# Performance work log

Measured on AMD Instinct MI355X. Metric: run time of the kernel, lower is better.

Reference implementation:

```python
import jax, jax.numpy as jnp
import numpy as np


def setup_inputs() -> dict:
    key = jax.random.key(0)
    k1, k2, k3, k4, k5 = jax.random.split(key, 5)
    B, D_IN, D_OUT = 8192, 4096, 4096
    inp = jax.random.normal(k1, (B, D_IN), dtype=jnp.float32)
    # dir_loc: kaiming-like init then row-normalized (as in __init__)
    dir_loc = jax.random.normal(k2, (D_OUT, D_IN), dtype=jnp.float32) * np.sqrt(2.0 / D_IN)
    dir_loc = dir_loc / jnp.sqrt(jnp.sum(dir_loc ** 2, axis=-1, keepdims=True))
    # raw (softplus-inverse) concentration parameter
    dir_conc_raw = jax.random.uniform(k3, (D_OUT,), dtype=jnp.float32) + 3.0
    # rad_layer = nn.Linear(in, out): default torch init ~ U(-1/sqrt(in), 1/sqrt(in))
    bound = 1.0 / np.sqrt(D_IN)
    rad_w = jax.random.uniform(k4, (D_OUT, D_IN), minval=-bound, maxval=bound, dtype=jnp.float32)
    rad_b = jax.random.uniform(k5, (D_OUT,), minval=-bound, maxval=bound, dtype=jnp.float32)
    bias = jnp.zeros((D_OUT,), dtype=jnp.float32)  # initialized uniform(0,0)
    return {"input": inp, "dir_loc": dir_loc, "dir_conc_raw": dir_conc_raw,
            "rad_w": rad_w, "rad_b": rad_b, "bias": bias}


def reference(input, dir_loc, dir_conc_raw, rad_w, rad_b, bias):
    # sample=False path: direction_sample = PowerSpherical(loc, kappa).mean
    #   = loc * kappa / (kappa + dim - 1), kappa = softplus(raw)
    d = dir_loc.shape[1]
    kappa = jax.nn.softplus(dir_conc_raw)                      # [O]
    direction = dir_loc * (kappa / (kappa + (d - 1)))[:, None]  # [O, I]
    # radius = softplus(Linear(input))
    radius = jax.nn.softplus(input @ rad_w.T + rad_b)          # [B, O]
    # (input.unsqueeze(1) * (direction * radius[..., None])).sum(-1) + bias
    # == (input @ direction.T) * radius + bias  (GEMM + elementwise scale)
    return (input @ direction.T) * radius + bias
```

## Files before the change

### kernel.cpp

```cpp
#include <hip/hip_runtime.h>
#include <hip/hip_bf16.h>
#include <math.h>


typedef __bf16 bf16x8 __attribute__((ext_vector_type(8)));
typedef float  f32x4  __attribute__((ext_vector_type(4)));
typedef unsigned short u16;
typedef u16   u16x4 __attribute__((ext_vector_type(4)));
typedef float f4    __attribute__((ext_vector_type(4)));

#define BDIM 8192
#define IDIM 4096
#define ODIM 4096
#define BM 256
#define BN 128
#define BK 32
#define NKT (IDIM/BK)

__device__ __forceinline__ u16 f2bf(float x){ __bf16 h=(__bf16)x; return __builtin_bit_cast(u16,h); }
__device__ __forceinline__ float bf2f(u16 u){ return (float)__builtin_bit_cast(__bf16,u); }

__global__ void k_scale(const float* __restrict__ raw, float* __restrict__ scale){
  int o = blockIdx.x*256 + threadIdx.x;
  if(o < ODIM){
    float x = raw[o];
    float k = (x > 20.f) ? x : log1pf(expf(x));
    scale[o] = k / (k + (float)(IDIM-1));
  }
}

__global__ void k_split(const f4* __restrict__ src, u16x4* __restrict__ hi,
                        u16x4* __restrict__ lo, int n4){
  int i = blockIdx.x*blockDim.x + threadIdx.x;
  int stride = gridDim.x*blockDim.x;
  for(; i<n4; i+=stride){
    f4 v = src[i];
    u16x4 h, l;
    #pragma unroll
    for(int j=0;j<4;++j){
      float x = v[j];
      u16 hb = f2bf(x);
      h[j] = hb;
      l[j] = f2bf(x - bf2f(hb));
    }
    hi[i]=h; lo[i]=l;
  }
}

__global__ void k_split_dir(const f4* __restrict__ src, const float* __restrict__ scale,
                            u16x4* __restrict__ hi, u16x4* __restrict__ lo, int n4){
  int i = blockIdx.x*blockDim.x + threadIdx.x;
  int stride = gridDim.x*blockDim.x;
  for(; i<n4; i+=stride){
    float s = scale[i>>10];
    f4 v = src[i];
    u16x4 h, l;
    #pragma unroll
    for(int j=0;j<4;++j){
      float x = v[j]*s;
      u16 hb = f2bf(x);
      h[j] = hb;
      l[j] = f2bf(x - bf2f(hb));
    }
    hi[i]=h; lo[i]=l;
  }
}

__device__ __forceinline__ void async16(const u16* g, u16* l){
  __builtin_amdgcn_global_load_lds((const __attribute__((address_space(1))) void*)g,
                                   (__attribute__((address_space(3))) void*)l, 16, 0, 0);
}

__global__ __launch_bounds__(512,2) void k_gemm(
    const u16* __restrict__ Ah, const u16* __restrict__ Al,
    const u16* __restrict__ Rh, const u16* __restrict__ Rl,
    const u16* __restrict__ Dh, const u16* __restrict__ Dl,
    const float* __restrict__ rad_b, const float* __restrict__ bias,
    float* __restrict__ out)
{
  __shared__ __align__(16) u16 smem[2*32768];

  const int tid  = threadIdx.x;
  const int lane = tid & 63;
  const int wid  = tid >> 6;
  const int wr = wid >> 1, wc = wid & 1;

  const int bid = blockIdx.x;
  const int swz = (bid & 7)*128 + (bid >> 3);
  const int bm = swz >> 5;
  const int bn = swz & 31;

  const int r0   = tid >> 2;
  const int cxor = (r0 >> 1) & 3;
  const int c0   = ((tid & 3) ^ cxor) * 8;
  const size_t arow = (size_t)(bm*BM + r0)*IDIM + c0;
  const size_t brow = (size_t)(bn*BN + r0)*IDIM + c0;
  const u16* gAh = Ah + arow;  const u16* gAl = Al + arow;
  const u16* gRh = Rh + brow;  const u16* gRl = Rl + brow;
  const u16* gDh = Dh + brow;  const u16* gDl = Dl + brow;
  u16* dst = smem + tid*8;

  const int lr   = lane & 15;
  const int koff = (((lane >> 4) ^ ((lr >> 1) & 3))) * 8;
  const int aoff = (wr*64 + lr)*BK + koff;
  const int boff = (wc*64 + lr)*BK + koff;

  f32x4 accR[4][4] = {};
  f32x4 accD[4][4] = {};

#define STAGE(BUF, KT) { \
    const int _ko = (KT)*BK; \
    u16* _d = dst + (BUF)*32768; \
    async16(gAh + _ko,            _d);         \
    async16(gAh + 128*IDIM + _ko, _d + 4096);  \
    async16(gAl + _ko,            _d + 8192);  \
    async16(gAl + 128*IDIM + _ko, _d + 12288); \
    async16(gRh + _ko,            _d + 16384); \
    async16(gRl + _ko,            _d + 20480); \
    async16(gDh + _ko,            _d + 24576); \
    async16(gDl + _ko,            _d + 28672); \
  }

#define COMPUTE(BUF) { \
    const u16* sb = smem + (BUF)*32768; \
    bf16x8 ah[4], al[4], bh[4], bl[4]; \
    _Pragma("unroll") for(int mi=0;mi<4;++mi){ \
      ah[mi] = *(const bf16x8*)(sb +        aoff + mi*512); \
      al[mi] = *(const bf16x8*)(sb + 8192 + aoff + mi*512); } \
    _Pragma("unroll") for(int ni=0;ni<4;++ni){ \
      bh[ni] = *(const bf16x8*)(sb + 16384 + boff + ni*512); \
      bl[ni] = *(const bf16x8*)(sb + 20480 + boff + ni*512); } \
    __builtin_amdgcn_s_setprio(1); \
    _Pragma("unroll") for(int mi=0;mi<4;++mi) \
      _Pragma("unroll") for(int ni=0;ni<4;++ni){ \
        accR[mi][ni] = __builtin_amdgcn_mfma_f32_16x16x32_bf16(ah[mi], bh[ni], accR[mi][ni],0,0,0); \
        accR[mi][ni] = __builtin_amdgcn_mfma_f32_16x16x32_bf16(ah[mi], bl[ni], accR[mi][ni],0,0,0); \
        accR[mi][ni] = __builtin_amdgcn_mfma_f32_16x16x32_bf16(al[mi], bh[ni], accR[mi][ni],0,0,0); } \
    __builtin_amdgcn_s_setprio(0); \
    _Pragma("unroll") for(int ni=0;ni<4;++ni){ \
      bh[ni] = *(const bf16x8*)(sb + 24576 + boff + ni*512); \
      bl[ni] = *(const bf16x8*)(sb + 28672 + boff + ni*512); } \
    __builtin_amdgcn_s_setprio(1); \
    _Pragma("unroll") for(int mi=0;mi<4;++mi) \
      _Pragma("unroll") for(int ni=0;ni<4;++ni){ \
        accD[mi][ni] = __builtin_amdgcn_mfma_f32_16x16x32_bf16(ah[mi], bh[ni], accD[mi][ni],0,0,0); \
        accD[mi][ni] = __builtin_amdgcn_mfma_f32_16x16x32_bf16(ah[mi], bl[ni], accD[mi][ni],0,0,0); \
        accD[mi][ni] = __builtin_amdgcn_mfma_f32_16x16x32_bf16(al[mi], bh[ni], accD[mi][ni],0,0,0); } \
    __builtin_amdgcn_s_setprio(0); \
  }

#define K_ITER(BUF, VM, DOSTAGE, NEXTK) { \
    asm volatile("s_waitcnt vmcnt(" VM ")" ::: "memory"); \
    __builtin_amdgcn_s_barrier(); \
    __builtin_amdgcn_sched_barrier(0); \
    COMPUTE(BUF); \
    asm volatile("s_waitcnt lgkmcnt(0)" ::: "memory"); \
    __builtin_amdgcn_sched_barrier(0); \
    __builtin_amdgcn_s_barrier(); \
    if (DOSTAGE) { STAGE(BUF, NEXTK) } \
    __builtin_amdgcn_sched_barrier(0); \
  }

  STAGE(0, 0)
  STAGE(1, 1)
  #pragma unroll 1
  for(int t=0; t<NKT-2; t+=2){
    K_ITER(0, "8", true, t+2)
    K_ITER(1, "8", true, t+3)
  }
  K_ITER(0, "8", false, 0)
  K_ITER(1, "0", false, 0)

#undef K_ITER
#undef COMPUTE
#undef STAGE

  const int orow0 = bm*BM + wr*64 + (lane>>4)*4;
  const int ocol0 = bn*BN + wc*64 + (lane & 15);
  #pragma unroll
  for(int ni=0;ni<4;++ni){
    const int col = ocol0 + ni*16;
    const float rb = rad_b[col];
    const float bs = bias[col];
    #pragma unroll
    for(int mi=0;mi<4;++mi){
      const int row = orow0 + mi*16;
      #pragma unroll
      for(int j=0;j<4;++j){
        float s  = accR[mi][ni][j] + rb;
        float sp = (s > 20.f) ? s : log1pf(expf(s));
        out[(size_t)(row+j)*ODIM + col] = accD[mi][ni][j]*sp + bs;
      }
    }
  }
}

extern "C" void kernel_launch(void* const* d_in, const int* in_sizes, int n_in,
                              void* d_out, int out_size, void* d_ws, size_t ws_size,
                              hipStream_t stream){
  (void)in_sizes; (void)n_in; (void)out_size; (void)ws_size;
  const float* inp  = (const float*)d_in[0];
  const float* dirl = (const float*)d_in[1];
  const float* draw = (const float*)d_in[2];
  const float* radw = (const float*)d_in[3];
  const float* radb = (const float*)d_in[4];
  const float* bias = (const float*)d_in[5];
  float* out = (float*)d_out;

  char* ws = (char*)d_ws;
  u16* Ah = (u16*)(ws);
  u16* Al = (u16*)(ws +  67108864L);
  u16* Rh = (u16*)(ws + 134217728L);
  u16* Rl = (u16*)(ws + 167772160L);
  u16* Dh = (u16*)(ws + 201326592L);
  u16* Dl = (u16*)(ws + 234881024L);
  float* scale = (float*)(ws + 268435456L);

  k_scale<<<dim3(ODIM/256), dim3(256), 0, stream>>>(draw, scale);

  const int n4A = BDIM*IDIM/4;
  const int n4W = ODIM*IDIM/4;
  k_split<<<dim3(2048), dim3(256), 0, stream>>>((const f4*)inp,  (u16x4*)Ah, (u16x4*)Al, n4A);
  k_split<<<dim3(2048), dim3(256), 0, stream>>>((const f4*)radw, (u16x4*)Rh, (u16x4*)Rl, n4W);
  k_split_dir<<<dim3(2048), dim3(256), 0, stream>>>((const f4*)dirl, scale, (u16x4*)Dh, (u16x4*)Dl, n4W);

  k_gemm<<<dim3((BDIM/BM)*(ODIM/BN)), dim3(512), 0, stream>>>(
      Ah, Al, Rh, Rl, Dh, Dl, radb, bias, out);
}
```

Baseline: 1.876 ms.

## Split each K tile into four MFMA phases interleaved with staged async loads

```diff
diff --git a/kernel.cpp b/kernel.cpp
--- a/kernel.cpp
+++ b/kernel.cpp
@@ -108,72 +108,124 @@
   f32x4 accR[4][4] = {};
   f32x4 accD[4][4] = {};
 
-#define STAGE(BUF, KT) { \
-    const int _ko = (KT)*BK; \
-    u16* _d = dst + (BUF)*32768; \
-    async16(gAh + _ko,            _d);         \
-    async16(gAh + 128*IDIM + _ko, _d + 4096);  \
-    async16(gAl + _ko,            _d + 8192);  \
-    async16(gAl + 128*IDIM + _ko, _d + 12288); \
-    async16(gRh + _ko,            _d + 16384); \
-    async16(gRl + _ko,            _d + 20480); \
-    async16(gDh + _ko,            _d + 24576); \
-    async16(gDl + _ko,            _d + 28672); \
-  }
-
-#define COMPUTE(BUF) { \
-    const u16* sb = smem + (BUF)*32768; \
-    bf16x8 ah[4], al[4], bh[4], bl[4]; \
-    _Pragma("unroll") for(int mi=0;mi<4;++mi){ \
-      ah[mi] = *(const bf16x8*)(sb +        aoff + mi*512); \
-      al[mi] = *(const bf16x8*)(sb + 8192 + aoff + mi*512); } \
-    _Pragma("unroll") for(int ni=0;ni<4;++ni){ \
-      bh[ni] = *(const bf16x8*)(sb + 16384 + boff + ni*512); \
-      bl[ni] = *(const bf16x8*)(sb + 20480 + boff + ni*512); } \
-    __builtin_amdgcn_s_setprio(1); \
-    _Pragma("unroll") for(int mi=0;mi<4;++mi) \
-      _Pragma("unroll") for(int ni=0;ni<4;++ni){ \
-        accR[mi][ni] = __builtin_amdgcn_mfma_f32_16x16x32_bf16(ah[mi], bh[ni], accR[mi][ni],0,0,0); \
-        accR[mi][ni] = __builtin_amdgcn_mfma_f32_16x16x32_bf16(ah[mi], bl[ni], accR[mi][ni],0,0,0); \
-        accR[mi][ni] = __builtin_amdgcn_mfma_f32_16x16x32_bf16(al[mi], bh[ni], accR[mi][ni],0,0,0); } \
-    __builtin_amdgcn_s_setprio(0); \
-    _Pragma("unroll") for(int ni=0;ni<4;++ni){ \
-      bh[ni] = *(const bf16x8*)(sb + 24576 + boff + ni*512); \
-      bl[ni] = *(const bf16x8*)(sb + 28672 + boff + ni*512); } \
-    __builtin_amdgcn_s_setprio(1); \
-    _Pragma("unroll") for(int mi=0;mi<4;++mi) \
-      _Pragma("unroll") for(int ni=0;ni<4;++ni){ \
-        accD[mi][ni] = __builtin_amdgcn_mfma_f32_16x16x32_bf16(ah[mi], bh[ni], accD[mi][ni],0,0,0); \
-        accD[mi][ni] = __builtin_amdgcn_mfma_f32_16x16x32_bf16(ah[mi], bl[ni], accD[mi][ni],0,0,0); \
-        accD[mi][ni] = __builtin_amdgcn_mfma_f32_16x16x32_bf16(al[mi], bh[ni], accD[mi][ni],0,0,0); } \
-    __builtin_amdgcn_s_setprio(0); \
-  }
-
-#define K_ITER(BUF, VM, DOSTAGE, NEXTK) { \
-    asm volatile("s_waitcnt vmcnt(" VM ")" ::: "memory"); \
-    __builtin_amdgcn_s_barrier(); \
-    __builtin_amdgcn_sched_barrier(0); \
-    COMPUTE(BUF); \
+#define MFMA16(A,B,C) __builtin_amdgcn_mfma_f32_16x16x32_bf16(A,B,C,0,0,0)
+
+#define STAGE_FULL(BUF, KT) { \
+    const int _k = (KT)*BK; \
+    u16* _df = dst + (BUF)*32768; \
+    async16(gAh + _k,            _df);         \
+    async16(gAh + 128*IDIM + _k, _df + 4096);  \
+    async16(gAl + _k,            _df + 8192);  \
+    async16(gAl + 128*IDIM + _k, _df + 12288); \
+    async16(gRh + _k,            _df + 16384); \
+    async16(gRl + _k,            _df + 20480); \
+    async16(gDh + _k,            _df + 24576); \
+    async16(gDl + _k,            _df + 28672); \
+  }
+
+#define PH_PRE  __builtin_amdgcn_s_barrier(); \
     asm volatile("s_waitcnt lgkmcnt(0)" ::: "memory"); \
     __builtin_amdgcn_sched_barrier(0); \
+    __builtin_amdgcn_s_setprio(1);
+#define PH_POST __builtin_amdgcn_s_setprio(0); \
     __builtin_amdgcn_s_barrier(); \
-    if (DOSTAGE) { STAGE(BUF, NEXTK) } \
-    __builtin_amdgcn_sched_barrier(0); \
-  }
-
-  STAGE(0, 0)
-  STAGE(1, 1)
+    __builtin_amdgcn_sched_barrier(0);
+
+#define K_TILE(BUF, VM, DOSTAGE, NEXTK) { \
+    const u16* sb = smem + (BUF)*32768; \
+    const int _ko = (NEXTK)*BK; \
+    u16* _d = dst + (BUF)*32768; \
+    bf16x8 ah[4], al[4]; \
+    {  \
+      bf16x8 b0[2], b1[2]; \
+      _Pragma("unroll") for(int mi=0;mi<4;++mi){ \
+        ah[mi] = *(const bf16x8*)(sb +        aoff + mi*512); \
+        al[mi] = *(const bf16x8*)(sb + 8192 + aoff + mi*512); } \
+      _Pragma("unroll") for(int ni=0;ni<2;++ni){ \
+        b0[ni] = *(const bf16x8*)(sb + 16384 + boff + ni*512); \
+        b1[ni] = *(const bf16x8*)(sb + 20480 + boff + ni*512); } \
+      PH_PRE \
+      _Pragma("unroll") for(int mi=0;mi<4;++mi) \
+        _Pragma("unroll") for(int ni=0;ni<2;++ni){ \
+          accR[mi][ni] = MFMA16(ah[mi], b0[ni], accR[mi][ni]); \
+          accR[mi][ni] = MFMA16(ah[mi], b1[ni], accR[mi][ni]); \
+          accR[mi][ni] = MFMA16(al[mi], b0[ni], accR[mi][ni]); } \
+      PH_POST \
+    } \
+    {  \
+      bf16x8 b0[2], b1[2]; \
+      _Pragma("unroll") for(int ni=0;ni<2;++ni){ \
+        b0[ni] = *(const bf16x8*)(sb + 16384 + boff + (ni+2)*512); \
+        b1[ni] = *(const bf16x8*)(sb + 20480 + boff + (ni+2)*512); } \
+      if (DOSTAGE) { \
+        async16(gAh + _ko,            _d);         \
+        async16(gAh + 128*IDIM + _ko, _d + 4096);  \
+        async16(gAl + _ko,            _d + 8192);  \
+        async16(gAl + 128*IDIM + _ko, _d + 12288); } \
+      PH_PRE \
+      _Pragma("unroll") for(int mi=0;mi<4;++mi) \
+        _Pragma("unroll") for(int ni=0;ni<2;++ni){ \
+          accR[mi][ni+2] = MFMA16(ah[mi], b0[ni], accR[mi][ni+2]); \
+          accR[mi][ni+2] = MFMA16(ah[mi], b1[ni], accR[mi][ni+2]); \
+          accR[mi][ni+2] = MFMA16(al[mi], b0[ni], accR[mi][ni+2]); } \
+      PH_POST \
+    } \
+    {  \
+      bf16x8 b0[2], b1[2]; \
+      _Pragma("unroll") for(int ni=0;ni<2;++ni){ \
+        b0[ni] = *(const bf16x8*)(sb + 24576 + boff + ni*512); \
+        b1[ni] = *(const bf16x8*)(sb + 28672 + boff + ni*512); } \
+      if (DOSTAGE) { \
+        async16(gRh + _ko, _d + 16384); \
+        async16(gRl + _ko, _d + 20480); } \
+      PH_PRE \
+      _Pragma("unroll") for(int mi=0;mi<4;++mi) \
+        _Pragma("unroll") for(int ni=0;ni<2;++ni){ \
+          accD[mi][ni] = MFMA16(ah[mi], b0[ni], accD[mi][ni]); \
+          accD[mi][ni] = MFMA16(ah[mi], b1[ni], accD[mi][ni]); \
+          accD[mi][ni] = MFMA16(al[mi], b0[ni], accD[mi][ni]); } \
+      PH_POST \
+    } \
+    {  \
+      bf16x8 b0[2], b1[2]; \
+      _Pragma("unroll") for(int ni=0;ni<2;++ni){ \
+        b0[ni] = *(const bf16x8*)(sb + 24576 + boff + (ni+2)*512); \
+        b1[ni] = *(const bf16x8*)(sb + 28672 + boff + (ni+2)*512); } \
+      PH_PRE \
+      _Pragma("unroll") for(int mi=0;mi<4;++mi) \
+        _Pragma("unroll") for(int ni=0;ni<2;++ni){ \
+          accD[mi][ni+2] = MFMA16(ah[mi], b0[ni], accD[mi][ni+2]); \
+          accD[mi][ni+2] = MFMA16(ah[mi], b1[ni], accD[mi][ni+2]); \
+          accD[mi][ni+2] = MFMA16(al[mi], b0[ni], accD[mi][ni+2]); } \
+      __builtin_amdgcn_s_setprio(0); \
+      asm volatile("s_waitcnt vmcnt(" VM ")" ::: "memory"); \
+      __builtin_amdgcn_s_barrier(); \
+      __builtin_amdgcn_sched_barrier(0); \
+      if (DOSTAGE) { \
+        async16(gDh + _ko, _d + 24576); \
+        async16(gDl + _ko, _d + 28672); } \
+    } \
+  }
+
+  STAGE_FULL(0, 0)
+  STAGE_FULL(1, 1)
+  asm volatile("s_waitcnt vmcnt(8)" ::: "memory");
+  __builtin_amdgcn_s_barrier();
+  __builtin_amdgcn_sched_barrier(0);
+
   #pragma unroll 1
   for(int t=0; t<NKT-2; t+=2){
-    K_ITER(0, "8", true, t+2)
-    K_ITER(1, "8", true, t+3)
-  }
-  K_ITER(0, "8", false, 0)
-  K_ITER(1, "0", false, 0)
-
-#undef K_ITER
-#undef COMPUTE
-#undef STAGE
+    K_TILE(0, "6", true, t+2)
+    K_TILE(1, "6", true, t+3)
+  }
+  K_TILE(0, "0", false, 0)
+  K_TILE(1, "0", false, 0)
+
+#undef K_TILE
+#undef PH_PRE
+#undef PH_POST
+#undef STAGE_FULL
+#undef MFMA16
 
   const int orow0 = bm*BM + wr*64 + (lane>>4)*4;
   const int ocol0 = bn*BN + wc*64 + (lane & 15);
```

New measurement: 1.815 ms. 1.03x faster.
